# Performance work log

Hardware: AMD Instinct MI355X
Metric: run time of the kernel (lower is better)

## Reference

```python
import jax, jax.numpy as jnp
import numpy as np

# --- static config (matches init_kwargs) ---
C = 384        # channels
H = 8          # num_heads
HD = C // H    # head_dim = 48
K = 1024       # patch_size (window)
BASE = 100.0   # rope_freq
MAX_POS = 4096
GRID_SIZE = 0.02
LN_EPS = 1e-5


def _interleave8(x, y, z):
    """Morton-interleave the low 8 bits of x,y,z -> 24-bit code (int32)."""
    key = jnp.zeros_like(x)
    for i in range(8):
        m = 1 << i
        key = key | ((x & m) << (2 * i + 2)) | ((y & m) << (2 * i + 1)) | ((z & m) << (2 * i))
    return key


def _serialize_points(xyz):
    """xyz: (B,3,N) -> (order (B,N) int32, grid (B,N,3) int32). Z-order sort."""
    pts = jnp.transpose(xyz, (0, 2, 1))                       # (B,N,3)
    grid = ((pts - pts.min(axis=1, keepdims=True)) / GRID_SIZE).astype(jnp.int32)
    grid = jnp.clip(grid, 0, 65535)
    gx, gy, gz = grid[..., 0], grid[..., 1], grid[..., 2]
    lo = _interleave8(gx & 255, gy & 255, gz & 255)           # low 24 bits of Morton code
    hi = _interleave8((gx >> 8) & 255, (gy >> 8) & 255, (gz >> 8) & 255)  # high word
    # 48-bit Morton order == lexsort with hi as primary key, lo secondary
    order = jax.vmap(lambda l, h: jnp.lexsort((l, h)))(lo, hi)
    return order.astype(jnp.int32), grid


def _rope_tables(d):
    inv_freq = 1.0 / (BASE ** (jnp.arange(0, d, 2, dtype=jnp.float32) / d))
    t = jnp.arange(MAX_POS, dtype=jnp.float32)
    freqs = t[:, None] * inv_freq[None, :]                    # (MAX_POS, d/2)
    freqs = jnp.concatenate([freqs, freqs], axis=-1)          # (MAX_POS, d)
    return jnp.cos(freqs), jnp.sin(freqs)


def _rotate_half(x):
    h = x.shape[-1] // 2
    return jnp.concatenate([-x[..., h:], x[..., :h]], axis=-1)


def _point_rope(tok, pos):
    """tok: (B,H,N,D) with D%3==0; pos: (B,N,3) int grid coords."""
    D = tok.shape[-1]
    d = D // 3
    pos = jnp.clip(pos, 0, MAX_POS - 1)
    cos, sin = _rope_tables(d)
    outs = []
    for axis, ch in enumerate(jnp.split(tok, 3, axis=-1)):
        p = pos[:, :, axis]                                   # (B,N)
        c = cos[p][:, None]                                   # (B,1,N,d)
        s = sin[p][:, None]
        outs.append(ch * c + _rotate_half(ch) * s)
    return jnp.concatenate(outs, axis=-1)


def _layernorm(x, g, b):
    mu = x.mean(axis=-1, keepdims=True)
    var = ((x - mu) ** 2).mean(axis=-1, keepdims=True)
    return (x - mu) * jax.lax.rsqrt(var + LN_EPS) * g + b


def _forward(x, xyz, ln1_g, ln1_b, qkv_w, qkv_b, proj_w, proj_b,
             ln2_g, ln2_b, ffn_w1, ffn_b1, ffn_w2, ffn_b2):
    B, C_, N = x.shape
    order, grid = _serialize_points(xyz)
    x_sorted = jnp.take_along_axis(x, order[:, None, :], axis=2)          # (B,C,N)
    grid_sorted = jnp.take_along_axis(grid, order[:, :, None], axis=1)    # (B,N,3)
    x_t = jnp.transpose(x_sorted, (0, 2, 1))                              # (B,N,C)
    shortcut = x_t
    xn = _layernorm(x_t, ln1_g, ln1_b)
    pad = (K - N % K) % K
    if pad > 0:
        xn = jnp.pad(xn, ((0, 0), (0, pad), (0, 0)))
        grid_sorted = jnp.pad(grid_sorted, ((0, 0), (0, pad), (0, 0)))
    Np = xn.shape[1]
    nw = Np // K
    qkv = (xn @ qkv_w + qkv_b).reshape(B, Np, 3, H, HD)
    q = jnp.transpose(qkv[:, :, 0], (0, 2, 1, 3))                         # (B,H,Np,HD)
    k = jnp.transpose(qkv[:, :, 1], (0, 2, 1, 3))
    v = jnp.transpose(qkv[:, :, 2], (0, 2, 1, 3))
    q = _point_rope(q, grid_sorted)
    k = _point_rope(k, grid_sorted)
    qw = q.reshape(B, H, nw, K, HD)
    kw = k.reshape(B, H, nw, K, HD)
    vw = v.reshape(B, H, nw, K, HD)
    scale = 1.0 / np.sqrt(HD).astype(np.float32)
    scores = jnp.einsum('bhwqd,bhwkd->bhwqk', qw, kw) * scale             # (B,H,nw,K,K)
    attn = jax.nn.softmax(scores, axis=-1)
    out = jnp.einsum('bhwqk,bhwkd->bhwqd', attn, vw)                      # (B,H,nw,K,HD)
    out = jnp.transpose(out, (0, 2, 3, 1, 4)).reshape(B, Np, C)
    out = out[:, :N]
    out = out @ proj_w + proj_b
    x_t = shortcut + out
    x_t = x_t + (jax.nn.gelu(_layernorm(x_t, ln2_g, ln2_b) @ ffn_w1 + ffn_b1,
                             approximate=False) @ ffn_w2 + ffn_b2)
    x_out = jnp.transpose(x_t, (0, 2, 1))                                 # (B,C,N)
    inv_order = jnp.argsort(order, axis=1)
    x_out = jnp.take_along_axis(x_out, inv_order[:, None, :], axis=2)
    return x_out


def setup_inputs() -> dict:
    key = jax.random.key(0)
    ks = jax.random.split(key, 12)
    B, N = 1, 16384
    s = 0.02
    return {
        'x': jax.random.normal(ks[0], (B, C, N), dtype=jnp.float32),
        'xyz': jax.random.uniform(ks[1], (B, 3, N), dtype=jnp.float32),
        'ln1_g': jnp.ones((C,), jnp.float32),
        'ln1_b': jnp.zeros((C,), jnp.float32),
        'qkv_w': jax.random.normal(ks[2], (C, 3 * C), jnp.float32) * s,
        'qkv_b': jnp.zeros((3 * C,), jnp.float32),
        'proj_w': jax.random.normal(ks[3], (C, C), jnp.float32) * s,
        'proj_b': jnp.zeros((C,), jnp.float32),
        'ln2_g': jnp.ones((C,), jnp.float32),
        'ln2_b': jnp.zeros((C,), jnp.float32),
        'ffn_w1': jax.random.normal(ks[4], (C, 4 * C), jnp.float32) * s,
        'ffn_b1': jnp.zeros((4 * C,), jnp.float32),
        'ffn_w2': jax.random.normal(ks[5], (4 * C, C), jnp.float32) * s,
        'ffn_b2': jnp.zeros((C,), jnp.float32),
    }


def reference(x, xyz, ln1_g, ln1_b, qkv_w, qkv_b, proj_w, proj_b,
              ln2_g, ln2_b, ffn_w1, ffn_b1, ffn_w2, ffn_b2):
    return _forward(x, xyz, ln1_g, ln1_b, qkv_w, qkv_b, proj_w, proj_b,
                    ln2_g, ln2_b, ffn_w1, ffn_b1, ffn_w2, ffn_b2)
```

## Files before the change

### kernel.cpp

```cpp
#include <hip/hip_runtime.h>
#include <hip/hip_bf16.h>

typedef unsigned short u16;
typedef unsigned int u32;
typedef unsigned long long u64;
typedef __attribute__((ext_vector_type(8))) short s16x8;
typedef __attribute__((ext_vector_type(4))) short s16x4;
typedef __attribute__((ext_vector_type(8))) unsigned short u16x8;
typedef __attribute__((ext_vector_type(4))) unsigned short u16x4;
typedef __attribute__((ext_vector_type(4))) float fx4;
typedef __attribute__((ext_vector_type(4))) unsigned int ux4;
typedef __attribute__((ext_vector_type(2))) unsigned int ux2;

__device__ __forceinline__ float bf2f(u16 u){ u32 x=((u32)u)<<16; return __builtin_bit_cast(float,x); }
__device__ __forceinline__ u16 f2bf(float f){ u32 x=__builtin_bit_cast(u32,f); return (u16)((x + 0x7FFFu + ((x>>16)&1u))>>16); }
__device__ __forceinline__ u32 cvtpk(float lo, float hi){
  u32 r; asm("v_cvt_pk_bf16_f32 %0, %1, %2" : "=v"(r) : "v"(lo), "v"(hi)); return r;
}

__device__ __forceinline__ s16x8 ld_bf8(const u16* p){
  s16x4 lo = *(const s16x4*)p;
  s16x4 hi = *(const s16x4*)(p+4);
  s16x8 r;
  r[0]=lo[0]; r[1]=lo[1]; r[2]=lo[2]; r[3]=lo[3];
  r[4]=hi[0]; r[5]=hi[1]; r[6]=hi[2]; r[7]=hi[3];
  return r;
}

__device__ __forceinline__ void gload16(const void* g, void* l){
  __builtin_amdgcn_global_load_lds((__attribute__((address_space(1))) void*)g,
                                   (__attribute__((address_space(3))) void*)l, 16, 0, 0);
}

__device__ __forceinline__ u64 spread3(u32 v){
  u64 x = v & 0xFFFFull;
  x = (x | (x<<32)) & 0x001f00000000ffffull;
  x = (x | (x<<16)) & 0x001f0000ff0000ffull;
  x = (x | (x<<8))  & 0x100f00f00f00f00full;
  x = (x | (x<<4))  & 0x10c30c30c30c30c3ull;
  x = (x | (x<<2))  & 0x1249249249249249ull;
  return x;
}

__global__ __launch_bounds__(256) void min3_kernel(const float* __restrict__ xyz, float* __restrict__ minsW, int N)
{
  __shared__ float red[3][4];
  int i = blockIdx.x*256 + threadIdx.x;
  int lane = threadIdx.x&63, wv = threadIdx.x>>6;
  float v0 = xyz[i], v1 = xyz[N+i], v2 = xyz[2*N+i];
  #pragma unroll
  for (int s=1;s<64;s<<=1){
    v0 = fminf(v0, __shfl_xor(v0,s));
    v1 = fminf(v1, __shfl_xor(v1,s));
    v2 = fminf(v2, __shfl_xor(v2,s));
  }
  if (lane==0){ red[0][wv]=v0; red[1][wv]=v1; red[2][wv]=v2; }
  __syncthreads();
  if (threadIdx.x < 3){
    float m = fminf(fminf(red[threadIdx.x][0],red[threadIdx.x][1]),
                    fminf(red[threadIdx.x][2],red[threadIdx.x][3]));
    minsW[blockIdx.x*3 + threadIdx.x] = m;
  }
}

__global__ __launch_bounds__(1024) void bsort_keys_kernel(const float* __restrict__ xyz, const float* __restrict__ minsW,
        u64* __restrict__ keys, int* __restrict__ gridO, int N)
{
  __shared__ u64 sk[2048];
  __shared__ float mnS[3];
  int t = threadIdx.x, bid = blockIdx.x;
  if (t < 192){
    float v = minsW[(t&63)*3 + (t>>6)];
    #pragma unroll
    for (int s=1;s<64;s<<=1) v = fminf(v, __shfl_xor(v,s));
    if ((t&63)==0) mnS[t>>6] = v;
  }
  __syncthreads();
  float mx0=mnS[0], mx1=mnS[1], mx2=mnS[2];
  int i0 = bid*2048;
  #pragma unroll
  for (int p=0;p<2;p++){
    int i = i0 + t + p*1024;
    int gx=(int)((xyz[i]-mx0)/0.02f);     gx = gx<0?0:(gx>65535?65535:gx);
    int gy=(int)((xyz[N+i]-mx1)/0.02f);   gy = gy<0?0:(gy>65535?65535:gy);
    int gz=(int)((xyz[2*N+i]-mx2)/0.02f); gz = gz<0?0:(gz>65535?65535:gz);
    gridO[i*3+0]=gx; gridO[i*3+1]=gy; gridO[i*3+2]=gz;
    u64 mort = (spread3((u32)gx)<<2)|(spread3((u32)gy)<<1)|spread3((u32)gz);
    sk[t + p*1024] = (mort<<14) | (u64)i;
  }
  for (int size=2; size<=2048; size<<=1){
    for (int stride=size>>1; stride>0; stride>>=1){
      __syncthreads();
      int i = 2*t - (t & (stride-1));
      int j = i + stride;
      u64 a = sk[i], b = sk[j];
      bool up = ((i & size) == 0);
      if ((a > b) == up){ sk[i]=b; sk[j]=a; }
    }
  }
  __syncthreads();
  keys[i0 + t] = sk[t];
  keys[i0 + 1024 + t] = sk[t+1024];
}

template<bool FINAL>
__global__ __launch_bounds__(256) void merge_kernel(const u64* __restrict__ src, u64* __restrict__ dst,
        int* __restrict__ order, int* __restrict__ iorder, int L, int N)
{
  int gt = blockIdx.x*256 + threadIdx.x;
  int d0 = gt*4;
  if (d0 >= N) return;
  int pair = d0 / (2*L);
  int base = pair*2*L;
  int ld = d0 - base;
  const u64* A = src + base;
  const u64* B = A + L;
  int lo = ld > L ? ld - L : 0;
  int hi = ld < L ? ld : L;
  while (lo < hi){
    int mid = (lo+hi)>>1;
    if (A[mid] <= B[ld-1-mid]) lo = mid+1; else hi = mid;
  }
  int i = lo, j = ld - lo;
  u64* out = dst + base + ld;
  int* oout = order + base + ld;
  u64 a = (i < L) ? A[i] : ~0ull;
  u64 b = (j < L) ? B[j] : ~0ull;
  #pragma unroll
  for (int e=0;e<4;e++){
    u64 v;
    if (a <= b){ v = a; i++; a = (i<L)?A[i]:~0ull; }
    else       { v = b; j++; b = (j<L)?B[j]:~0ull; }
    out[e] = v;
    if (FINAL){
      int orig = (int)(v & 16383ull);
      oout[e] = orig;
      iorder[orig] = base + ld + e;
    }
  }
}

__global__ __launch_bounds__(256) void wtrans4_kernel(const float* __restrict__ qkv_w, const float* __restrict__ proj_w,
    const float* __restrict__ w1, const float* __restrict__ w2,
    u16* __restrict__ qkv_wT, u16* __restrict__ proj_wT, u16* __restrict__ w1T, u16* __restrict__ w2T)
{
  __shared__ float tl[32][33];
  int bid = blockIdx.x;
  const float* W; u16* Wt; int K, Nc, lb;
  if (bid < 432)      { W=qkv_w;  Wt=qkv_wT;  K=384;  Nc=1152; lb=bid; }
  else if (bid < 576) { W=proj_w; Wt=proj_wT; K=384;  Nc=384;  lb=bid-432; }
  else if (bid < 1152){ W=w1;     Wt=w1T;     K=384;  Nc=1536; lb=bid-576; }
  else                { W=w2;     Wt=w2T;     K=1536; Nc=384;  lb=bid-1152; }
  int nb = Nc/32;
  int n0 = (lb % nb)*32;
  int k0 = (lb / nb)*32;
  int t=threadIdx.x; int r=t>>5, c=t&31;
  #pragma unroll
  for (int p=0;p<4;p++) tl[p*8+r][c] = W[(size_t)(k0+p*8+r)*Nc + n0+c];
  __syncthreads();
  #pragma unroll
  for (int p=0;p<4;p++) Wt[(size_t)(n0+p*8+r)*K + k0+c] = f2bf(tl[c][p*8+r]);
}

template<bool BF16IN>
__global__ __launch_bounds__(256) void ln32_kernel(const void* __restrict__ xin, const float* __restrict__ g,
     const float* __restrict__ b, u16* __restrict__ xn, int N)
{
  extern __shared__ char dsm[];
  float* tile = (float*)dsm;
  int n0 = blockIdx.x*32;
  int t = threadIdx.x;
  int tok32 = t&31, cg2 = t>>5;
  #pragma unroll 8
  for (int p=0;p<48;p++){
    int cc = p*8 + cg2;
    float v;
    if (BF16IN) v = bf2f(((const u16*)xin)[(size_t)cc*N + n0 + tok32]);
    else        v = ((const float*)xin)[(size_t)cc*N + n0 + tok32];
    tile[tok32*388 + cc] = v;
  }
  __syncthreads();
  int tok = t>>3, part = t&7;
  const float* row = tile + tok*388 + part*48;
  float s=0.f;
  #pragma unroll
  for (int j=0;j<48;j++) s += row[j];
  s += __shfl_xor(s,1); s += __shfl_xor(s,2); s += __shfl_xor(s,4);
  float mu = s*(1.0f/384.0f);
  float vr=0.f;
  #pragma unroll
  for (int j=0;j<48;j++){ float d=row[j]-mu; vr += d*d; }
  vr += __shfl_xor(vr,1); vr += __shfl_xor(vr,2); vr += __shfl_xor(vr,4);
  float rs = rsqrtf(vr*(1.0f/384.0f) + 1e-5f);
  u16* dst = xn + (size_t)(n0+tok)*384 + part*48;
  #pragma unroll
  for (int q=0;q<6;q++){
    float v[8];
    #pragma unroll
    for (int j=0;j<8;j++){
      int c = part*48 + q*8 + j;
      v[j] = (row[q*8+j]-mu)*rs*g[c] + b[c];
    }
    ux4 o;
    o[0]=cvtpk(v[0],v[1]); o[1]=cvtpk(v[2],v[3]); o[2]=cvtpk(v[4],v[5]); o[3]=cvtpk(v[6],v[7]);
    *(ux4*)(dst + q*8) = o;
  }
}

__device__ __forceinline__ float gelu_f(float v){
  return 0.5f*v*(1.0f + erff(v*0.7071067811865475f));
}

#define LOG2_100_O8 0.8304820237218405f

__global__ __launch_bounds__(512) void gemm256qkv_kernel(const u16* __restrict__ A, const u16* __restrict__ Bt,
    const float* __restrict__ bias, const int* __restrict__ iorder, const int* __restrict__ gridO,
    u16* __restrict__ Qp, u16* __restrict__ Kp, u16* __restrict__ Vp, int M, int K)
{
  __shared__ u16 Al[256*64];
  __shared__ u16 Bl[128*64];
  int nmt = M>>8;
  int m0 = (blockIdx.x % nmt)<<8;
  int n0 = (blockIdx.x / nmt)<<7;
  int t = threadIdx.x, lane=t&63, wv=t>>6, wr=wv>>1, wc=wv&1;
  int fr = lane&15, fg = lane>>4;
  fx4 acc[4][4];
  #pragma unroll
  for (int i=0;i<4;i++)
  #pragma unroll
  for (int j=0;j<4;j++) acc[i][j]=(fx4){0.f,0.f,0.f,0.f};
  int srowA = wv*32 + (lane>>3);
  int srowB = wv*16 + (lane>>3);
  int swz  = ((lane&7) ^ ((lane>>3)&7)) * 8;
  const u16* ApL = A  + (size_t)(m0+srowA)*K + swz;
  const u16* BpL = Bt + (size_t)(n0+srowB)*K + swz;
  u16* AlW = Al + wv*2048 + lane*8;
  u16* BlW = Bl + wv*1024 + lane*8;
  const u16* a_base = Al + (wr*64+fr)*64;
  const u16* b_base = Bl + (wc*64+fr)*64;
  int swr = fr & 7;
  for (int k0=0;k0<K;k0+=64){
    #pragma unroll
    for (int i=0;i<4;i++) gload16(ApL + k0 + (size_t)i*8*K, AlW + i*512);
    #pragma unroll
    for (int i=0;i<2;i++) gload16(BpL + k0 + (size_t)i*8*K, BlW + i*512);
    __syncthreads();
    #pragma unroll
    for (int ks=0;ks<2;ks++){
      int soff = (((ks*4+fg) ^ swr) << 3);
      s16x8 a[4], b[4];
      #pragma unroll
      for (int mi=0;mi<4;mi++) a[mi] = *(const s16x8*)(a_base + mi*1024 + soff);
      #pragma unroll
      for (int ni=0;ni<4;ni++) b[ni] = *(const s16x8*)(b_base + ni*1024 + soff);
      #pragma unroll
      for (int mi=0;mi<4;mi++)
      #pragma unroll
      for (int ni=0;ni<4;ni++)
        acc[mi][ni] = __builtin_amdgcn_mfma_f32_16x16x32_bf16(a[mi], b[ni], acc[mi][ni], 0,0,0);
    }
    __syncthreads();
  }
  float invf = __builtin_amdgcn_exp2f(-(float)(fr&7) * LOG2_100_O8);
  bool hiLane = (fr & 8) != 0;
  #pragma unroll
  for (int mi=0;mi<4;mi++){
    int tokb = m0 + wr*64 + mi*16 + fg*4;
    int io4[4];
    #pragma unroll
    for (int j=0;j<4;j++) io4[j] = iorder[tokb+j];
    #pragma unroll
    for (int ni=0;ni<4;ni++){
      int c = n0 + wc*64 + ni*16 + fr;
      float bi = bias[c];
      int sec = c/384;
      int rem = c - sec*384;
      int h = rem/48;
      int a = (rem%48)>>4;
      u16* dst = (sec==0) ? Qp : ((sec==1) ? Kp : Vp);
      #pragma unroll
      for (int j=0;j<4;j++){
        float v = acc[mi][ni][j] + bi;
        float outv;
        if (sec < 2){
          int pos = gridO[(tokb+j)*3 + a];
          pos = pos>4095?4095:pos;
          float ang = (float)pos * invf;
          float cs = __cosf(ang), sn = __sinf(ang);
          float p = __shfl_xor(v, 8);
          outv = hiLane ? (v*cs + p*sn) : (v*cs - p*sn);
        } else {
          outv = v;
        }
        dst[((size_t)h*M + io4[j])*48 + a*16 + fr] = f2bf(outv);
      }
    }
  }
}

template<int EPI>
__global__ __launch_bounds__(512) void gemm256_kernel(const u16* __restrict__ A, const u16* __restrict__ Bt,
    const float* __restrict__ bias, u16* __restrict__ outB, int M, int Nout, int K)
{
  __shared__ u16 Al[256*64];
  __shared__ u16 Bl[128*64];
  int nmt = M>>8;
  int m0 = (blockIdx.x % nmt)<<8;
  int n0 = (blockIdx.x / nmt)<<7;
  int t = threadIdx.x, lane=t&63, wv=t>>6, wr=wv>>1, wc=wv&1;
  int fr = lane&15, fg = lane>>4;
  fx4 acc[4][4];
  #pragma unroll
  for (int i=0;i<4;i++)
  #pragma unroll
  for (int j=0;j<4;j++) acc[i][j]=(fx4){0.f,0.f,0.f,0.f};
  int srowA = wv*32 + (lane>>3);
  int srowB = wv*16 + (lane>>3);
  int swz  = ((lane&7) ^ ((lane>>3)&7)) * 8;
  const u16* ApL = A  + (size_t)(m0+srowA)*K + swz;
  const u16* BpL = Bt + (size_t)(n0+srowB)*K + swz;
  u16* AlW = Al + wv*2048 + lane*8;
  u16* BlW = Bl + wv*1024 + lane*8;
  const u16* a_base = Al + (wr*64+fr)*64;
  const u16* b_base = Bl + (wc*64+fr)*64;
  int swr = fr & 7;
  for (int k0=0;k0<K;k0+=64){
    #pragma unroll
    for (int i=0;i<4;i++) gload16(ApL + k0 + (size_t)i*8*K, AlW + i*512);
    #pragma unroll
    for (int i=0;i<2;i++) gload16(BpL + k0 + (size_t)i*8*K, BlW + i*512);
    __syncthreads();
    #pragma unroll
    for (int ks=0;ks<2;ks++){
      int soff = (((ks*4+fg) ^ swr) << 3);
      s16x8 a[4], b[4];
      #pragma unroll
      for (int mi=0;mi<4;mi++) a[mi] = *(const s16x8*)(a_base + mi*1024 + soff);
      #pragma unroll
      for (int ni=0;ni<4;ni++) b[ni] = *(const s16x8*)(b_base + ni*1024 + soff);
      #pragma unroll
      for (int mi=0;mi<4;mi++)
      #pragma unroll
      for (int ni=0;ni<4;ni++)
        acc[mi][ni] = __builtin_amdgcn_mfma_f32_16x16x32_bf16(a[mi], b[ni], acc[mi][ni], 0,0,0);
    }
    __syncthreads();
  }
  #pragma unroll
  for (int mi=0;mi<4;mi++)
  #pragma unroll
  for (int ni=0;ni<4;ni++){
    int c = n0 + wc*64 + ni*16 + fr;
    float bi = bias[c];
    int mb = m0 + wr*64 + mi*16 + fg*4;
    #pragma unroll
    for (int j=0;j<4;j++){
      float vv = acc[mi][ni][j] + bi;
      if (EPI==1) vv = gelu_f(vv);
      outB[(size_t)(mb+j)*Nout + c] = f2bf(vv);
    }
  }
}

template<int EPI>
__global__ __launch_bounds__(256) void gemm128x2_kernel(const u16* __restrict__ A, const u16* __restrict__ Bt,
    const float* __restrict__ bias, u16* __restrict__ outB, float* __restrict__ outF,
    const float* __restrict__ resF, const u16* __restrict__ resB, int M, int Nout, int K)
{
  __shared__ u16 Al[2][128*64];
  __shared__ u16 Bl[2][128*64];
  int nmt = M>>7;
  int m0 = (blockIdx.x % nmt)<<7;
  int n0 = (blockIdx.x / nmt)<<7;
  int t = threadIdx.x, lane=t&63, wv=t>>6, wr=wv>>1, wc=wv&1;
  int fr = lane&15, fg = lane>>4;
  fx4 acc[4][4];
  #pragma unroll
  for (int i=0;i<4;i++)
  #pragma unroll
  for (int j=0;j<4;j++) acc[i][j]=(fx4){0.f,0.f,0.f,0.f};
  int srow = wv*32 + (lane>>3);
  int swz  = ((lane&7) ^ ((lane>>3)&7)) * 8;
  const u16* ApL = A  + (size_t)(m0+srow)*K + swz;
  const u16* BpL = Bt + (size_t)(n0+srow)*K + swz;
  int woff = wv*2048 + lane*8;
  int swr = fr & 7;
  for (int k0=0;k0<K;k0+=128){
    #pragma unroll
    for (int i=0;i<4;i++){
      gload16(ApL + k0 +      (size_t)i*8*K, Al[0] + woff + i*512);
      gload16(BpL + k0 +      (size_t)i*8*K, Bl[0] + woff + i*512);
      gload16(ApL + k0 + 64 + (size_t)i*8*K, Al[1] + woff + i*512);
      gload16(BpL + k0 + 64 + (size_t)i*8*K, Bl[1] + woff + i*512);
    }
    __syncthreads();
    #pragma unroll
    for (int sub=0;sub<2;sub++){
      const u16* a_base = Al[sub] + (wr*64+fr)*64;
      const u16* b_base = Bl[sub] + (wc*64+fr)*64;
      #pragma unroll
      for (int ks=0;ks<2;ks++){
        int soff = (((ks*4+fg) ^ swr) << 3);
        s16x8 a[4], b[4];
        #pragma unroll
        for (int mi=0;mi<4;mi++) a[mi] = *(const s16x8*)(a_base + mi*1024 + soff);
        #pragma unroll
        for (int ni=0;ni<4;ni++) b[ni] = *(const s16x8*)(b_base + ni*1024 + soff);
        #pragma unroll
        for (int mi=0;mi<4;mi++)
        #pragma unroll
        for (int ni=0;ni<4;ni++)
          acc[mi][ni] = __builtin_amdgcn_mfma_f32_16x16x32_bf16(a[mi], b[ni], acc[mi][ni], 0,0,0);
      }
    }
    __syncthreads();
  }
  if (EPI==2){
    #pragma unroll
    for (int mi=0;mi<4;mi++)
    #pragma unroll
    for (int ni=0;ni<4;ni++){
      int c = n0 + wc*64 + ni*16 + fr;
      float bi = bias[c];
      size_t idx = (size_t)c*M + m0 + wr*64 + mi*16 + fg*4;
      fx4 r4 = *(const fx4*)(resF + idx);
      ux2 p;
      p[0] = cvtpk(acc[mi][ni][0]+bi+r4[0], acc[mi][ni][1]+bi+r4[1]);
      p[1] = cvtpk(acc[mi][ni][2]+bi+r4[2], acc[mi][ni][3]+bi+r4[3]);
      *(ux2*)(outB + idx) = p;
    }
  } else {
    #pragma unroll
    for (int mi=0;mi<4;mi++)
    #pragma unroll
    for (int ni=0;ni<4;ni++){
      int c = n0 + wc*64 + ni*16 + fr;
      float bi = bias[c];
      size_t idx = (size_t)c*M + m0 + wr*64 + mi*16 + fg*4;
      ux2 rb = *(const ux2*)(resB + idx);
      fx4 o;
      o[0] = acc[mi][ni][0] + bi + bf2f((u16)rb[0]);
      o[1] = acc[mi][ni][1] + bi + bf2f((u16)(rb[0]>>16));
      o[2] = acc[mi][ni][2] + bi + bf2f((u16)rb[1]);
      o[3] = acc[mi][ni][3] + bi + bf2f((u16)(rb[1]>>16));
      *(fx4*)(outF + idx) = o;
    }
  }
}

#define ATTN_SCALE 0.14433756729740643f
#define E2SCALE 0.2082354550504211f
#define DEFER_RAW 55.0f
#define KSTRIDE 68

__global__ __launch_bounds__(512) void attn7_kernel(const u16* __restrict__ Qp, const u16* __restrict__ Kp,
    const u16* __restrict__ Vp, const int* __restrict__ order, u16* __restrict__ attn, int N, int nw)
{
  __shared__ u16 Kl[2][64*KSTRIDE];
  __shared__ u16 Vl[2][48*KSTRIDE];
  __shared__ u16 Pl[8][32*KSTRIDE];
  int b = blockIdx.x;
  int hw = b & 127;
  int qc = b >> 7;
  int w = hw % nw, h = hw / nw;
  int t = threadIdx.x, lane = t&63, wv = t>>6;
  int fr = lane & 15, fg = lane >> 4;
  size_t base = ((size_t)h*N + (size_t)w*1024);
  int q0 = qc*256 + wv*32;
  bool kact = t < 384;
  int krow = t/6, kc = t - krow*6;
  const u16* ksrc = Kp + (base + krow)*48 + kc*8;
  int koff = krow*KSTRIDE + kc*8;
  int s2 = t - 128;
  bool vact = t >= 128;
  int vrow = s2/6, vc = s2 - vrow*6;
  const u16* vsrc = Vp + (base + vrow)*48 + vc*8;
  int vkey = vrow ^ (vc<<3);
  if (t < 256){
    ux2 z = {0,0};
    *(ux2*)&Kl[0][(t>>2)*KSTRIDE + 48 + (t&3)*4] = z;
    *(ux2*)&Kl[1][(t>>2)*KSTRIDE + 48 + (t&3)*4] = z;
  }
  s16x8 qf[2][2];
  s16x8 zf = {0,0,0,0,0,0,0,0};
  #pragma unroll
  for (int n=0;n<2;n++){
    const u16* qrow = Qp + (base + q0 + n*16 + fr)*48;
    qf[n][0] = ld_bf8(qrow + fg*8);
    qf[n][1] = (fg < 2) ? ld_bf8(qrow + 32 + fg*8) : zf;
  }
  s16x8 ones;
  #pragma unroll
  for (int j=0;j<8;j++) ones[j] = (short)0x3F80;

  float m0r = -3.4e38f, m1r = -3.4e38f;
  fx4 o00=(fx4){0.f,0.f,0.f,0.f}, o01=o00, o02=o00, o03=o00, o10=o00, o11=o00, o12=o00, o13=o00;
  u16* pl = Pl[wv];
  ux4 kreg = {0,0,0,0}, vreg = {0,0,0,0};
  if (kact) kreg = *(const ux4*)ksrc;
  if (vact) vreg = *(const ux4*)vsrc;
  if (kact){
    ux2 lo; lo[0]=kreg[0]; lo[1]=kreg[1];
    ux2 hi; hi[0]=kreg[2]; hi[1]=kreg[3];
    *(ux2*)(Kl[0]+koff) = lo; *(ux2*)(Kl[0]+koff+4) = hi;
  }
  if (vact){
    u16* vcp = Vl[0] + vkey;
    vcp[(vc*8+0)*KSTRIDE] = (u16)vreg[0];
    vcp[(vc*8+1)*KSTRIDE] = (u16)(vreg[0]>>16);
    vcp[(vc*8+2)*KSTRIDE] = (u16)vreg[1];
    vcp[(vc*8+3)*KSTRIDE] = (u16)(vreg[1]>>16);
    vcp[(vc*8+4)*KSTRIDE] = (u16)vreg[2];
    vcp[(vc*8+5)*KSTRIDE] = (u16)(vreg[2]>>16);
    vcp[(vc*8+6)*KSTRIDE] = (u16)vreg[3];
    vcp[(vc*8+7)*KSTRIDE] = (u16)(vreg[3]>>16);
  }
  __syncthreads();

  for (int c=0;c<16;c++){
    int cur = c & 1;
    const u16* kl = Kl[cur];
    const u16* vl = Vl[cur];
    if (c < 15){
      if (kact) kreg = *(const ux4*)(ksrc + (size_t)(c+1)*3072);
      if (vact) vreg = *(const ux4*)(vsrc + (size_t)(c+1)*3072);
    }
    fx4 s0[4], s1v[4];
    __builtin_amdgcn_s_setprio(1);
    #pragma unroll
    for (int m=0;m<4;m++){
      s0[m]=(fx4){0.f,0.f,0.f,0.f}; s1v[m]=s0[m];
      #pragma unroll
      for (int s=0;s<2;s++){
        s16x8 af = ld_bf8(kl + (m*16+fr)*KSTRIDE + s*32 + fg*8);
        s0[m]  = __builtin_amdgcn_mfma_f32_16x16x32_bf16(af, qf[0][s], s0[m],  0,0,0);
        s1v[m] = __builtin_amdgcn_mfma_f32_16x16x32_bf16(af, qf[1][s], s1v[m], 0,0,0);
      }
    }
    __builtin_amdgcn_s_setprio(0);
    float pm0 = -3.4e38f, pm1 = -3.4e38f;
    #pragma unroll
    for (int m=0;m<4;m++){
      float a0 = fmaxf(fmaxf(s0[m][0],s0[m][1]), fmaxf(s0[m][2],s0[m][3]));
      float a1 = fmaxf(fmaxf(s1v[m][0],s1v[m][1]), fmaxf(s1v[m][2],s1v[m][3]));
      pm0 = fmaxf(pm0, a0); pm1 = fmaxf(pm1, a1);
    }
    pm0 = fmaxf(pm0, __shfl_xor(pm0,16)); pm0 = fmaxf(pm0, __shfl_xor(pm0,32));
    pm1 = fmaxf(pm1, __shfl_xor(pm1,16)); pm1 = fmaxf(pm1, __shfl_xor(pm1,32));
    if (!__all((pm0 <= m0r + DEFER_RAW) & (pm1 <= m1r + DEFER_RAW))){
      float nm0 = fmaxf(m0r, pm0), nm1 = fmaxf(m1r, pm1);
      float f0 = __builtin_amdgcn_exp2f((m0r - nm0)*E2SCALE);
      float f1 = __builtin_amdgcn_exp2f((m1r - nm1)*E2SCALE);
      m0r = nm0; m1r = nm1;
      #pragma unroll
      for (int j=0;j<4;j++){
        float g0 = __shfl(f0, fg*4+j);
        float g1 = __shfl(f1, fg*4+j);
        o00[j]*=g0; o01[j]*=g0; o02[j]*=g0; o03[j]*=g0;
        o10[j]*=g1; o11[j]*=g1; o12[j]*=g1; o13[j]*=g1;
      }
    }
    #pragma unroll
    for (int m=0;m<4;m++){
      float e0[4], e1[4];
      #pragma unroll
      for (int j=0;j<4;j++){
        e0[j] = __builtin_amdgcn_exp2f((s0[m][j]-m0r)*E2SCALE);
        e1[j] = __builtin_amdgcn_exp2f((s1v[m][j]-m1r)*E2SCALE);
      }
      ux2 P0, P1;
      P0[0]=cvtpk(e0[0],e0[1]); P0[1]=cvtpk(e0[2],e0[3]);
      P1[0]=cvtpk(e1[0],e1[1]); P1[1]=cvtpk(e1[2],e1[3]);
      *(ux2*)&pl[(fr)*KSTRIDE + m*16 + fg*4]      = P0;
      *(ux2*)&pl[(16+fr)*KSTRIDE + m*16 + fg*4]   = P1;
    }
    __builtin_amdgcn_s_setprio(1);
    #pragma unroll
    for (int s=0;s<2;s++){
      int kb = s*32 + fg*8;
      s16x8 pa0 = ld_bf8(pl + fr*KSTRIDE + kb);
      s16x8 pa1 = ld_bf8(pl + (16+fr)*KSTRIDE + kb);
      s16x8 vb0 = ld_bf8(vl + (fr)*KSTRIDE    + (kb ^ ((fr)&56)));
      s16x8 vb1 = ld_bf8(vl + (16+fr)*KSTRIDE + (kb ^ ((16+fr)&56)));
      s16x8 vb2 = ld_bf8(vl + (32+fr)*KSTRIDE + (kb ^ ((32+fr)&56)));
      o00 = __builtin_amdgcn_mfma_f32_16x16x32_bf16(pa0, vb0, o00, 0,0,0);
      o01 = __builtin_amdgcn_mfma_f32_16x16x32_bf16(pa0, vb1, o01, 0,0,0);
      o02 = __builtin_amdgcn_mfma_f32_16x16x32_bf16(pa0, vb2, o02, 0,0,0);
      o03 = __builtin_amdgcn_mfma_f32_16x16x32_bf16(pa0, ones, o03, 0,0,0);
      o10 = __builtin_amdgcn_mfma_f32_16x16x32_bf16(pa1, vb0, o10, 0,0,0);
      o11 = __builtin_amdgcn_mfma_f32_16x16x32_bf16(pa1, vb1, o11, 0,0,0);
      o12 = __builtin_amdgcn_mfma_f32_16x16x32_bf16(pa1, vb2, o12, 0,0,0);
      o13 = __builtin_amdgcn_mfma_f32_16x16x32_bf16(pa1, ones, o13, 0,0,0);
    }
    __builtin_amdgcn_s_setprio(0);
    if (c < 15){
      u16* kln = Kl[cur^1];
      u16* vln = Vl[cur^1];
      if (kact){
        ux2 lo; lo[0]=kreg[0]; lo[1]=kreg[1];
        ux2 hi; hi[0]=kreg[2]; hi[1]=kreg[3];
        *(ux2*)(kln+koff) = lo; *(ux2*)(kln+koff+4) = hi;
      }
      if (vact){
        u16* vcp = vln + vkey;
        vcp[(vc*8+0)*KSTRIDE] = (u16)vreg[0];
        vcp[(vc*8+1)*KSTRIDE] = (u16)(vreg[0]>>16);
        vcp[(vc*8+2)*KSTRIDE] = (u16)vreg[1];
        vcp[(vc*8+3)*KSTRIDE] = (u16)(vreg[1]>>16);
        vcp[(vc*8+4)*KSTRIDE] = (u16)vreg[2];
        vcp[(vc*8+5)*KSTRIDE] = (u16)(vreg[2]>>16);
        vcp[(vc*8+6)*KSTRIDE] = (u16)vreg[3];
        vcp[(vc*8+7)*KSTRIDE] = (u16)(vreg[3]>>16);
      }
      __syncthreads();
    }
  }
  const int* ord = order + w*1024 + q0;
  #pragma unroll
  for (int j=0;j<4;j++){
    float inv0 = 1.0f / o03[j];
    float inv1 = 1.0f / o13[j];
    int orig0 = ord[fg*4+j];
    u16* dst0 = attn + (size_t)orig0*384 + h*48;
    dst0[fr]      = f2bf(o00[j]*inv0);
    dst0[16+fr]   = f2bf(o01[j]*inv0);
    dst0[32+fr]   = f2bf(o02[j]*inv0);
    int orig1 = ord[16 + fg*4+j];
    u16* dst1 = attn + (size_t)orig1*384 + h*48;
    dst1[fr]      = f2bf(o10[j]*inv1);
    dst1[16+fr]   = f2bf(o11[j]*inv1);
    dst1[32+fr]   = f2bf(o12[j]*inv1);
  }
}

extern "C" void kernel_launch(void* const* d_in, const int* in_sizes, int n_in,
                              void* d_out, int out_size, void* d_ws, size_t ws_size,
                              hipStream_t stream)
{
  (void)n_in; (void)out_size; (void)ws_size;
  const float* x     = (const float*)d_in[0];
  const float* xyz   = (const float*)d_in[1];
  const float* ln1_g = (const float*)d_in[2];
  const float* ln1_b = (const float*)d_in[3];
  const float* qkv_w = (const float*)d_in[4];
  const float* qkv_b = (const float*)d_in[5];
  const float* proj_w= (const float*)d_in[6];
  const float* proj_b= (const float*)d_in[7];
  const float* ln2_g = (const float*)d_in[8];
  const float* ln2_b = (const float*)d_in[9];
  const float* ffn_w1= (const float*)d_in[10];
  const float* ffn_b1= (const float*)d_in[11];
  const float* ffn_w2= (const float*)d_in[12];
  const float* ffn_b2= (const float*)d_in[13];
  int N = in_sizes[0]/384;
  int nw = N/1024;
  char* wsp = (char*)d_ws;
  size_t off = 0;
  auto alloc = [&](size_t bytes)->char*{ char* p = wsp + off; off = (off + bytes + 255) & ~(size_t)255; return p; };
  int*  order   = (int*)alloc((size_t)N*4);
  int*  iorder  = (int*)alloc((size_t)N*4);
  int*  gridO   = (int*)alloc((size_t)N*12);
  float* minsW  = (float*)alloc((size_t)(N/256)*12);
  u64*  keysA   = (u64*)alloc((size_t)N*8);
  u64*  keysB   = (u64*)alloc((size_t)N*8);
  u16*  qkv_wT  = (u16*)alloc((size_t)1152*384*2);
  u16*  proj_wT = (u16*)alloc((size_t)384*384*2);
  u16*  w1T     = (u16*)alloc((size_t)1536*384*2);
  u16*  w2T     = (u16*)alloc((size_t)384*1536*2);
  u16*  xn      = (u16*)alloc((size_t)N*384*2);
  u16*  Qp      = (u16*)alloc((size_t)N*48*8*2);
  u16*  Kp      = (u16*)alloc((size_t)N*48*8*2);
  u16*  Vp      = (u16*)alloc((size_t)N*48*8*2);
  u16*  xn2     = (u16*)alloc((size_t)N*384*2);
  u16*  y1b     = (u16*)alloc((size_t)N*384*2);
  u16*  attn    = xn;
  u16*  mid     = xn;
  float* outF = (float*)d_out;

  min3_kernel<<<N/256, 256, 0, stream>>>(xyz, minsW, N);
  bsort_keys_kernel<<<N/2048, 1024, 0, stream>>>(xyz, minsW, keysA, gridO, N);
  merge_kernel<false><<<N/1024, 256, 0, stream>>>(keysA, keysB, order, iorder, 2048, N);
  merge_kernel<false><<<N/1024, 256, 0, stream>>>(keysB, keysA, order, iorder, 4096, N);
  merge_kernel<true><<<N/1024, 256, 0, stream>>>(keysA, keysB, order, iorder, 8192, N);

  wtrans4_kernel<<<1728, 256, 0, stream>>>(qkv_w, proj_w, ffn_w1, ffn_w2, qkv_wT, proj_wT, w1T, w2T);
  ln32_kernel<false><<<N/32, 256, 32*388*4, stream>>>(x, ln1_g, ln1_b, xn, N);
  gemm256qkv_kernel<<<(N/256)*(1152/128), 512, 0, stream>>>(xn, qkv_wT, qkv_b, iorder, gridO, Qp, Kp, Vp, N, 384);
  attn7_kernel<<<8*nw*4, 512, 0, stream>>>(Qp, Kp, Vp, order, attn, N, nw);
  gemm128x2_kernel<2><<<(N/128)*(384/128), 256, 0, stream>>>(attn, proj_wT, proj_b, y1b, nullptr, x, nullptr, N, 384, 384);
  ln32_kernel<true><<<N/32, 256, 32*388*4, stream>>>(y1b, ln2_g, ln2_b, xn2, N);
  gemm256_kernel<1><<<(N/256)*(1536/128), 512, 0, stream>>>(xn2, w1T, ffn_b1, mid, N, 1536, 384);
  gemm128x2_kernel<3><<<(N/128)*(384/128), 256, 0, stream>>>(mid, w2T, ffn_b2, nullptr, outF, nullptr, y1b, N, 384, 1536);
}
```

Baseline: 245.4 us.

## Double-buffer K-loop in 128x128 GEMMs and shrink bitonic sort blocks

```diff
diff --git a/kernel.cpp b/kernel.cpp
--- a/kernel.cpp
+++ b/kernel.cpp
@@ -63,10 +63,10 @@
   }
 }
 
-__global__ __launch_bounds__(1024) void bsort_keys_kernel(const float* __restrict__ xyz, const float* __restrict__ minsW,
+__global__ __launch_bounds__(512) void bsort_keys_kernel(const float* __restrict__ xyz, const float* __restrict__ minsW,
         u64* __restrict__ keys, int* __restrict__ gridO, int N)
 {
-  __shared__ u64 sk[2048];
+  __shared__ u64 sk[1024];
   __shared__ float mnS[3];
   int t = threadIdx.x, bid = blockIdx.x;
   if (t < 192){
@@ -77,18 +77,18 @@
   }
   __syncthreads();
   float mx0=mnS[0], mx1=mnS[1], mx2=mnS[2];
-  int i0 = bid*2048;
+  int i0 = bid*1024;
   #pragma unroll
   for (int p=0;p<2;p++){
-    int i = i0 + t + p*1024;
+    int i = i0 + t + p*512;
     int gx=(int)((xyz[i]-mx0)/0.02f);     gx = gx<0?0:(gx>65535?65535:gx);
     int gy=(int)((xyz[N+i]-mx1)/0.02f);   gy = gy<0?0:(gy>65535?65535:gy);
     int gz=(int)((xyz[2*N+i]-mx2)/0.02f); gz = gz<0?0:(gz>65535?65535:gz);
     gridO[i*3+0]=gx; gridO[i*3+1]=gy; gridO[i*3+2]=gz;
     u64 mort = (spread3((u32)gx)<<2)|(spread3((u32)gy)<<1)|spread3((u32)gz);
-    sk[t + p*1024] = (mort<<14) | (u64)i;
-  }
-  for (int size=2; size<=2048; size<<=1){
+    sk[t + p*512] = (mort<<14) | (u64)i;
+  }
+  for (int size=2; size<=1024; size<<=1){
     for (int stride=size>>1; stride>0; stride>>=1){
       __syncthreads();
       int i = 2*t - (t & (stride-1));
@@ -100,7 +100,7 @@
   }
   __syncthreads();
   keys[i0 + t] = sk[t];
-  keys[i0 + 1024 + t] = sk[t+1024];
+  keys[i0 + 512 + t] = sk[t+512];
 }
 
 template<bool FINAL>
@@ -363,7 +363,7 @@
 }
 
 template<int EPI>
-__global__ __launch_bounds__(256) void gemm128x2_kernel(const u16* __restrict__ A, const u16* __restrict__ Bt,
+__global__ __launch_bounds__(256) void gemm128p_kernel(const u16* __restrict__ A, const u16* __restrict__ Bt,
     const float* __restrict__ bias, u16* __restrict__ outB, float* __restrict__ outF,
     const float* __restrict__ resF, const u16* __restrict__ resB, int M, int Nout, int K)
 {
@@ -385,33 +385,38 @@
   const u16* BpL = Bt + (size_t)(n0+srow)*K + swz;
   int woff = wv*2048 + lane*8;
   int swr = fr & 7;
-  for (int k0=0;k0<K;k0+=128){
-    #pragma unroll
-    for (int i=0;i<4;i++){
-      gload16(ApL + k0 +      (size_t)i*8*K, Al[0] + woff + i*512);
-      gload16(BpL + k0 +      (size_t)i*8*K, Bl[0] + woff + i*512);
-      gload16(ApL + k0 + 64 + (size_t)i*8*K, Al[1] + woff + i*512);
-      gload16(BpL + k0 + 64 + (size_t)i*8*K, Bl[1] + woff + i*512);
-    }
-    __syncthreads();
-    #pragma unroll
-    for (int sub=0;sub<2;sub++){
-      const u16* a_base = Al[sub] + (wr*64+fr)*64;
-      const u16* b_base = Bl[sub] + (wc*64+fr)*64;
-      #pragma unroll
-      for (int ks=0;ks<2;ks++){
-        int soff = (((ks*4+fg) ^ swr) << 3);
-        s16x8 a[4], b[4];
-        #pragma unroll
-        for (int mi=0;mi<4;mi++) a[mi] = *(const s16x8*)(a_base + mi*1024 + soff);
-        #pragma unroll
-        for (int ni=0;ni<4;ni++) b[ni] = *(const s16x8*)(b_base + ni*1024 + soff);
-        #pragma unroll
-        for (int mi=0;mi<4;mi++)
-        #pragma unroll
-        for (int ni=0;ni<4;ni++)
-          acc[mi][ni] = __builtin_amdgcn_mfma_f32_16x16x32_bf16(a[mi], b[ni], acc[mi][ni], 0,0,0);
+  #pragma unroll
+  for (int i=0;i<4;i++){
+    gload16(ApL + (size_t)i*8*K, Al[0] + woff + i*512);
+    gload16(BpL + (size_t)i*8*K, Bl[0] + woff + i*512);
+  }
+  __syncthreads();
+  int niter = K>>6;
+  for (int it=0; it<niter; ++it){
+    int cur = it & 1;
+    if (it+1 < niter){
+      int k1 = (it+1)<<6;
+      #pragma unroll
+      for (int i=0;i<4;i++){
+        gload16(ApL + k1 + (size_t)i*8*K, Al[cur^1] + woff + i*512);
+        gload16(BpL + k1 + (size_t)i*8*K, Bl[cur^1] + woff + i*512);
       }
+    }
+    const u16* a_base = Al[cur] + (wr*64+fr)*64;
+    const u16* b_base = Bl[cur] + (wc*64+fr)*64;
+    #pragma unroll
+    for (int ks=0;ks<2;ks++){
+      int soff = (((ks*4+fg) ^ swr) << 3);
+      s16x8 a[4], b[4];
+      #pragma unroll
+      for (int mi=0;mi<4;mi++) a[mi] = *(const s16x8*)(a_base + mi*1024 + soff);
+      #pragma unroll
+      for (int ni=0;ni<4;ni++) b[ni] = *(const s16x8*)(b_base + ni*1024 + soff);
+      #pragma unroll
+      for (int mi=0;mi<4;mi++)
+      #pragma unroll
+      for (int ni=0;ni<4;ni++)
+        acc[mi][ni] = __builtin_amdgcn_mfma_f32_16x16x32_bf16(a[mi], b[ni], acc[mi][ni], 0,0,0);
     }
     __syncthreads();
   }
@@ -678,17 +683,18 @@
   float* outF = (float*)d_out;
 
   min3_kernel<<<N/256, 256, 0, stream>>>(xyz, minsW, N);
-  bsort_keys_kernel<<<N/2048, 1024, 0, stream>>>(xyz, minsW, keysA, gridO, N);
-  merge_kernel<false><<<N/1024, 256, 0, stream>>>(keysA, keysB, order, iorder, 2048, N);
-  merge_kernel<false><<<N/1024, 256, 0, stream>>>(keysB, keysA, order, iorder, 4096, N);
-  merge_kernel<true><<<N/1024, 256, 0, stream>>>(keysA, keysB, order, iorder, 8192, N);
+  bsort_keys_kernel<<<N/1024, 512, 0, stream>>>(xyz, minsW, keysA, gridO, N);
+  merge_kernel<false><<<N/1024, 256, 0, stream>>>(keysA, keysB, order, iorder, 1024, N);
+  merge_kernel<false><<<N/1024, 256, 0, stream>>>(keysB, keysA, order, iorder, 2048, N);
+  merge_kernel<false><<<N/1024, 256, 0, stream>>>(keysA, keysB, order, iorder, 4096, N);
+  merge_kernel<true><<<N/1024, 256, 0, stream>>>(keysB, keysA, order, iorder, 8192, N);
 
   wtrans4_kernel<<<1728, 256, 0, stream>>>(qkv_w, proj_w, ffn_w1, ffn_w2, qkv_wT, proj_wT, w1T, w2T);
   ln32_kernel<false><<<N/32, 256, 32*388*4, stream>>>(x, ln1_g, ln1_b, xn, N);
   gemm256qkv_kernel<<<(N/256)*(1152/128), 512, 0, stream>>>(xn, qkv_wT, qkv_b, iorder, gridO, Qp, Kp, Vp, N, 384);
   attn7_kernel<<<8*nw*4, 512, 0, stream>>>(Qp, Kp, Vp, order, attn, N, nw);
-  gemm128x2_kernel<2><<<(N/128)*(384/128), 256, 0, stream>>>(attn, proj_wT, proj_b, y1b, nullptr, x, nullptr, N, 384, 384);
+  gemm128p_kernel<2><<<(N/128)*(384/128), 256, 0, stream>>>(attn, proj_wT, proj_b, y1b, nullptr, x, nullptr, N, 384, 384);
   ln32_kernel<true><<<N/32, 256, 32*388*4, stream>>>(y1b, ln2_g, ln2_b, xn2, N);
   gemm256_kernel<1><<<(N/256)*(1536/128), 512, 0, stream>>>(xn2, w1T, ffn_b1, mid, N, 1536, 384);
-  gemm128x2_kernel<3><<<(N/128)*(384/128), 256, 0, stream>>>(mid, w2T, ffn_b2, nullptr, outF, nullptr, y1b, N, 384, 1536);
-}
+  gemm128p_kernel<3><<<(N/128)*(384/128), 256, 0, stream>>>(mid, w2T, ffn_b2, nullptr, outF, nullptr, y1b, N, 384, 1536);
+}
```

Result: no change. 247.0 us (+0.6%).
